# Optimization experiments

Measured on AMD Instinct MI355X. Metric: run time of the kernel, lower is better.

The kernel has to match this reference:

```python
import jax, jax.numpy as jnp
import numpy as np

D = 18          # belief dimension (max category dim)
EPS = 0.1       # C.eps
PROP_STEP = 5   # C.prop_step
CC = 0.01       # label-injection constant c in forward
DIM_A = 4       # category_dim_dict['author']
DIM_P = 18      # category_dim_dict['paper']


def _init_belief(mask, label, dim, d):
    # X[tr_idx] = -c everywhere, then X[tr_idx, label] += dim*c
    m = (mask != 0).astype(jnp.float32)[:, None]            # [N,1]
    X = -CC * m + (dim * CC) * m * jax.nn.one_hot(label, d, dtype=jnp.float32)
    col_mask = (jnp.arange(d) < dim).astype(jnp.float32)    # zero cols >= dim
    Y = X * col_mask
    return X, Y, col_mask


def setup_inputs() -> dict:
    key = jax.random.key(0)
    ks = jax.random.split(key, 8)
    E, NA, NP = 2_000_000, 100_000, 500_000
    return {
        "H_ap": jax.random.normal(ks[0], (D, D), dtype=jnp.float32),
        "H_pa": jax.random.normal(ks[1], (D, D), dtype=jnp.float32),
        "w": jnp.ones((E,), dtype=jnp.float32),
        "edge_src": jax.random.randint(ks[2], (E,), 0, NA, dtype=jnp.int32),
        "edge_dst": jax.random.randint(ks[3], (E,), 0, NP, dtype=jnp.int32),
        "train_mask_a": jax.random.randint(ks[4], (NA,), 0, 2, dtype=jnp.int32),
        "label_a": jax.random.randint(ks[5], (NA,), 0, DIM_A, dtype=jnp.int32),
        "train_mask_p": jax.random.randint(ks[6], (NP,), 0, 2, dtype=jnp.int32),
        "label_p": jax.random.randint(ks[7], (NP,), 0, DIM_P, dtype=jnp.int32),
        "n_author": NA,
        "n_paper": NP,
    }


def reference(H_ap, H_pa, w, edge_src, edge_dst, train_mask_a, label_a,
              train_mask_p, label_p, n_author, n_paper):
    # Belief init via scatter-based label injection (per node type)
    Xa, Ya, cm_a = _init_belief(train_mask_a, label_a, DIM_A, D)
    Xp, Yp, cm_p = _init_belief(train_mask_p, label_p, DIM_P, D)

    seg = jax.ops.segment_sum
    for _ in range(PROP_STEP):  # ZooBP residual updates over hetero edge types
        # author -> paper: gather, transform by H_ap, weighted scatter-add
        msg_p = seg(w[:, None] * (Ya[edge_src] @ H_ap), edge_dst,
                    num_segments=n_paper)                       # [NP, D]
        # paper -> author (inverse etype, H_pa ~ H_ap^T structure)
        msg_a = seg(w[:, None] * (Yp[edge_dst] @ H_pa), edge_src,
                    num_segments=n_author)                      # [NA, D]
        Ya = (Xa + (EPS / D) * msg_a) * cm_a
        Yp = (Xp + (EPS / D) * msg_p) * cm_p
    return Ya, Yp
```

## Files before the change

### kernel.cpp

```cpp
#include <hip/hip_runtime.h>


static constexpr int   DD     = 18;
static constexpr int   DIMA   = 4;
static constexpr float CCF    = 0.01f;
static constexpr float SCALEF = 0.1f / 18.0f;
static constexpr int   PROP   = 5;

static constexpr int NBLK  = 512;
static constexpr int BT    = 512;
static constexpr int PSH   = 10;
static constexpr int ASH   = 9;
static constexpr int PBK   = 512;
static constexpr int ABK   = 256;
static constexpr int PNB   = 1 << PSH;
static constexpr int ANB   = 1 << ASH;
static constexpr int NBIN  = PBK + ABK;
static constexpr int NBINS = NBIN * NBLK;

__device__ __forceinline__ float bf2f(unsigned short u) {
    return __uint_as_float(((unsigned int)u) << 16);
}
__device__ __forceinline__ unsigned short f2bf(float f) {
    unsigned int x = __float_as_uint(f);
    return (unsigned short)((x + 0x7fffu + ((x >> 16) & 1u)) >> 16);
}
__device__ __forceinline__ unsigned int f2w13(float f) {
    unsigned int x = __float_as_uint(f);
    return ((x + 0x3ffffu + ((x >> 19) & 1u)) >> 19) & 0x1fffu;
}
__device__ __forceinline__ float w132f(unsigned int u) {
    return __uint_as_float(u << 19);
}
__device__ __forceinline__ int swz_blk() {
    return ((int)blockIdx.x & 7) * (NBLK >> 3) + ((int)blockIdx.x >> 3);
}

__global__ __launch_bounds__(BT) void count_bins(
    const int* __restrict__ esrc, const int* __restrict__ edst,
    int* __restrict__ bb, int E, int chunk)
{
    __shared__ int hP[PBK];
    __shared__ int hA[ABK];
    int t = threadIdx.x, b = swz_blk();
    if (t < PBK) hP[t] = 0;
    if (t < ABK) hA[t] = 0;
    __syncthreads();
    int beg = b * chunk;
    int end = beg + chunk; if (end > E) end = E;
    for (int e = beg + t; e < end; e += BT) {
        atomicAdd(&hP[edst[e] >> PSH], 1);
        atomicAdd(&hA[esrc[e] >> ASH], 1);
    }
    __syncthreads();
    if (t < PBK) bb[t * NBLK + b] = hP[t];
    if (t < ABK) bb[(PBK + t) * NBLK + b] = hA[t];
}

__global__ __launch_bounds__(256) void scan_block(
    int* __restrict__ off, int* __restrict__ bsum, int NT)
{
    __shared__ int s[256];
    int t = threadIdx.x;
    int i = blockIdx.x * 256 + t;
    int v = (i < NT) ? off[i] : 0;
    s[t] = v; __syncthreads();
    for (int dlt = 1; dlt < 256; dlt <<= 1) {
        int x = (t >= dlt) ? s[t - dlt] : 0;
        __syncthreads();
        s[t] += x;
        __syncthreads();
    }
    if (i < NT) off[i] = s[t] - v;
    if (t == 255) bsum[blockIdx.x] = s[255];
}

__global__ __launch_bounds__(256) void scan_tops(int* __restrict__ bsum, int nb)
{
    __shared__ int s[256];
    int t = threadIdx.x;
    int K = (nb + 255) / 256;
    int base = t * K;
    int sum = 0;
    for (int r = 0; r < K; ++r) { int idx = base + r; if (idx < nb) sum += bsum[idx]; }
    s[t] = sum; __syncthreads();
    for (int dlt = 1; dlt < 256; dlt <<= 1) {
        int x = (t >= dlt) ? s[t - dlt] : 0;
        __syncthreads();
        s[t] += x;
        __syncthreads();
    }
    int run = s[t] - sum;
    for (int r = 0; r < K; ++r) {
        int idx = base + r;
        if (idx < nb) { int tmp = bsum[idx]; bsum[idx] = run; run += tmp; }
    }
}

__global__ __launch_bounds__(BT) void scat_p(
    const int* __restrict__ esrc, const int* __restrict__ edst,
    const float* __restrict__ w, const int* __restrict__ bb,
    const int* __restrict__ bsum, uint2* __restrict__ S, int E, int chunk)
{
    __shared__ int base[PBK];
    int t = threadIdx.x, b = swz_blk();
    if (t < PBK) {
        int idx = t * NBLK + b;
        base[t] = bb[idx] + bsum[idx >> 8];
    }
    __syncthreads();
    int beg = b * chunk;
    int end = beg + chunk; if (end > E) end = E;
    for (int e = beg + t; e < end; e += BT) {
        int d = edst[e], s = esrc[e];
        unsigned int rec = ((unsigned int)s << 13) | f2w13(w[e]);
        int pos = atomicAdd(&base[d >> PSH], 1);
        S[pos] = make_uint2(rec, (unsigned int)(d & (PNB - 1)));
    }
}

__global__ __launch_bounds__(BT) void scat_a(
    const int* __restrict__ esrc, const int* __restrict__ edst,
    const float* __restrict__ w, const int* __restrict__ bb,
    const int* __restrict__ bsum, uint2* __restrict__ S, int E, int chunk,
    int NPH)
{
    __shared__ int base[ABK];
    int t = threadIdx.x, b = swz_blk();
    if (t < ABK) {
        int idx = (PBK + t) * NBLK + b;
        base[t] = bb[idx] + bsum[idx >> 8] - E;
    }
    __syncthreads();
    int beg = b * chunk;
    int end = beg + chunk; if (end > E) end = E;
    for (int e = beg + t; e < end; e += BT) {
        int d = edst[e], s = esrc[e];
        unsigned int rec = ((unsigned int)d << 13) | f2w13(w[e]);
        unsigned int key = ((unsigned int)(s & (ANB - 1)) << 1) | (d >= NPH ? 1u : 0u);
        int pos = atomicAdd(&base[s >> ASH], 1);
        S[pos] = make_uint2(rec, key);
    }
}

__global__ __launch_bounds__(BT) void csr_p(
    const int* __restrict__ bb, const int* __restrict__ bsum,
    const uint2* __restrict__ S,
    unsigned int* __restrict__ adjP, int* __restrict__ offP, int NP, int E)
{
    __shared__ int c[PNB];
    __shared__ int loc[PNB];
    __shared__ int ps[BT];
    int t = threadIdx.x, b = blockIdx.x;
    int i0 = b * NBLK;
    int i1 = (b + 1) * NBLK;
    int sbeg = bb[i0] + bsum[i0 >> 8];
    int send = bb[i1] + bsum[i1 >> 8];
    for (int i = t; i < PNB; i += BT) c[i] = 0;
    __syncthreads();
    for (int i = sbeg + t; i < send; i += BT)
        atomicAdd(&c[S[i].y], 1);
    __syncthreads();
    int a[2]; int sum = 0;
#pragma unroll
    for (int k = 0; k < 2; ++k) { a[k] = c[t * 2 + k]; sum += a[k]; }
    ps[t] = sum; __syncthreads();
    for (int dlt = 1; dlt < BT; dlt <<= 1) {
        int x = (t >= dlt) ? ps[t - dlt] : 0;
        __syncthreads();
        ps[t] += x;
        __syncthreads();
    }
    int run = ps[t] - sum;
    int n0 = (b << PSH) + t * 2;
#pragma unroll
    for (int k = 0; k < 2; ++k) {
        loc[t * 2 + k] = run;
        if (n0 + k < NP) offP[n0 + k] = sbeg + run;
        run += a[k];
    }
    if (b == 0 && t == 0) offP[NP] = E;
    __syncthreads();
    for (int i = sbeg + t; i < send; i += BT) {
        uint2 r = S[i];
        int p = atomicAdd(&loc[r.y], 1);
        adjP[sbeg + p] = r.x;
    }
}

__global__ __launch_bounds__(BT) void csr_a_init(
    const int* __restrict__ bb, const int* __restrict__ bsum,
    const uint2* __restrict__ S,
    unsigned int* __restrict__ adjA, int* __restrict__ offA,
    const int* __restrict__ mask_a, const int* __restrict__ lab_a,
    const int* __restrict__ mask_p, const int* __restrict__ lab_p,
    const float* __restrict__ Hpa,
    ushort4* __restrict__ Ya, ushort4* __restrict__ Zp,
    unsigned char* __restrict__ priorA, unsigned char* __restrict__ priorP,
    int NA, int NTot, int E)
{
    if ((int)blockIdx.x < ABK) {
        __shared__ int c[2 * ANB];
        __shared__ int loc[2 * ANB];
        __shared__ int ps[BT];
        int t = threadIdx.x, b = blockIdx.x;
        int x0 = (PBK + b) * NBLK;
        int sbeg = bb[x0] + bsum[x0 >> 8] - E;
        int send;
        if (b == ABK - 1) send = E;
        else { int x1 = x0 + NBLK; send = bb[x1] + bsum[x1 >> 8] - E; }
        for (int i = t; i < 2 * ANB; i += BT) c[i] = 0;
        __syncthreads();
        for (int i = sbeg + t; i < send; i += BT)
            atomicAdd(&c[S[i].y], 1);
        __syncthreads();
        int a2[2]; int sum = 0;
#pragma unroll
        for (int k = 0; k < 2; ++k) { a2[k] = c[t * 2 + k]; sum += a2[k]; }
        ps[t] = sum; __syncthreads();
        for (int dlt = 1; dlt < BT; dlt <<= 1) {
            int x = (t >= dlt) ? ps[t - dlt] : 0;
            __syncthreads();
            ps[t] += x;
            __syncthreads();
        }
        int run = ps[t] - sum;
        int n0 = (b << (ASH + 1)) + t * 2;
#pragma unroll
        for (int k = 0; k < 2; ++k) {
            loc[t * 2 + k] = run;
            if (n0 + k < 2 * NA) offA[n0 + k] = sbeg + run;
            run += a2[k];
        }
        if (b == 0 && t == 0) offA[2 * NA] = E;
        __syncthreads();
        for (int i = sbeg + t; i < send; i += BT) {
            uint2 r = S[i];
            int p = atomicAdd(&loc[r.y], 1);
            adjA[sbeg + p] = r.x;
        }
    } else {
        __shared__ float sH[72], sCol[4];
        int t = threadIdx.x;
        if (t < 72) sH[t] = Hpa[(t >> 2) * DD + (t & 3)];
        if (t < 4) { float s = 0.f; for (int k = 0; k < DD; ++k) s += Hpa[k * DD + t]; sCol[t] = s; }
        __syncthreads();
        int i = ((int)blockIdx.x - ABK) * BT + t;
        if (i >= NTot) return;
        if (i < NA) {
            float x[4] = {0.f, 0.f, 0.f, 0.f};
            int m = mask_a[i];
            int l = m ? lab_a[i] : 0;
            if (m) {
                x[0] = x[1] = x[2] = x[3] = -CCF;
                x[l] += (float)DIMA * CCF;
            }
            priorA[i] = m ? (unsigned char)(0x20 | l) : 0;
            Ya[i] = make_ushort4(f2bf(x[0]), f2bf(x[1]), f2bf(x[2]), f2bf(x[3]));
        } else {
            int d = i - NA;
            float z0 = 0.f, z1 = 0.f, z2 = 0.f, z3 = 0.f;
            int m = mask_p[d];
            int l = m ? lab_p[d] : 0;
            if (m) {
                float lb = (float)DD * CCF;
                z0 = -CCF * sCol[0] + lb * sH[l * 4 + 0];
                z1 = -CCF * sCol[1] + lb * sH[l * 4 + 1];
                z2 = -CCF * sCol[2] + lb * sH[l * 4 + 2];
                z3 = -CCF * sCol[3] + lb * sH[l * 4 + 3];
            }
            priorP[d] = m ? (unsigned char)(0x20 | l) : 0;
            Zp[d] = make_ushort4(f2bf(z0), f2bf(z1), f2bf(z2), f2bf(z3));
        }
    }
}

__global__ __launch_bounds__(256) void gather_iter(
    const int* __restrict__ offP, const int* __restrict__ offA,
    const unsigned int* __restrict__ adjP, const unsigned int* __restrict__ adjA,
    const ushort4* __restrict__ ZpOld, ushort4* __restrict__ ZpNew,
    const ushort4* __restrict__ YaOld, ushort4* __restrict__ YaNew,
    const unsigned char* __restrict__ priorA, const unsigned char* __restrict__ priorP,
    const float* __restrict__ Hap, const float* __restrict__ Hpa,
    float* __restrict__ out, int NP, int NA, int last, int gpB)
{
    if ((int)blockIdx.x < gpB) {
        __shared__ float sH[72], sCol[4], sM[16], sHap[72];
        int t = threadIdx.x;
        if (t < 72) sH[t] = Hpa[(t >> 2) * DD + (t & 3)];
        if (t < 4) { float s = 0.f; for (int k = 0; k < DD; ++k) s += Hpa[k * DD + t]; sCol[t] = s; }
        if (t < 16) { int i = t >> 2, j = t & 3; float s = 0.f;
                      for (int k = 0; k < DD; ++k) s += Hap[i * DD + k] * Hpa[k * DD + j];
                      sM[t] = SCALEF * s; }
        if (t < 72) sHap[t] = SCALEF * Hap[t];
        __syncthreads();

        int d = (int)blockIdx.x * 256 + t;
        if (d >= NP) return;
        int beg = offP[d], end = offP[d + 1];
        unsigned int pb = priorP[d];
        float ax = 0.f, ay = 0.f, az = 0.f, aw = 0.f;
        int s = beg;
        for (; s + 8 <= end; s += 8) {
            unsigned int e0 = adjP[s],     e1 = adjP[s + 1], e2 = adjP[s + 2], e3 = adjP[s + 3];
            unsigned int e4 = adjP[s + 4], e5 = adjP[s + 5], e6 = adjP[s + 6], e7 = adjP[s + 7];
            ushort4 y0 = YaOld[e0 >> 13], y1 = YaOld[e1 >> 13];
            ushort4 y2 = YaOld[e2 >> 13], y3 = YaOld[e3 >> 13];
            ushort4 y4 = YaOld[e4 >> 13], y5 = YaOld[e5 >> 13];
            ushort4 y6 = YaOld[e6 >> 13], y7 = YaOld[e7 >> 13];
            float w0 = w132f(e0 & 0x1fffu), w1 = w132f(e1 & 0x1fffu);
            float w2 = w132f(e2 & 0x1fffu), w3 = w132f(e3 & 0x1fffu);
            float w4 = w132f(e4 & 0x1fffu), w5 = w132f(e5 & 0x1fffu);
            float w6 = w132f(e6 & 0x1fffu), w7 = w132f(e7 & 0x1fffu);
            ax += w0 * bf2f(y0.x) + w1 * bf2f(y1.x) + w2 * bf2f(y2.x) + w3 * bf2f(y3.x)
                + w4 * bf2f(y4.x) + w5 * bf2f(y5.x) + w6 * bf2f(y6.x) + w7 * bf2f(y7.x);
            ay += w0 * bf2f(y0.y) + w1 * bf2f(y1.y) + w2 * bf2f(y2.y) + w3 * bf2f(y3.y)
                + w4 * bf2f(y4.y) + w5 * bf2f(y5.y) + w6 * bf2f(y6.y) + w7 * bf2f(y7.y);
            az += w0 * bf2f(y0.z) + w1 * bf2f(y1.z) + w2 * bf2f(y2.z) + w3 * bf2f(y3.z)
                + w4 * bf2f(y4.z) + w5 * bf2f(y5.z) + w6 * bf2f(y6.z) + w7 * bf2f(y7.z);
            aw += w0 * bf2f(y0.w) + w1 * bf2f(y1.w) + w2 * bf2f(y2.w) + w3 * bf2f(y3.w)
                + w4 * bf2f(y4.w) + w5 * bf2f(y5.w) + w6 * bf2f(y6.w) + w7 * bf2f(y7.w);
        }
        for (; s + 4 <= end; s += 4) {
            unsigned int e0 = adjP[s], e1 = adjP[s + 1], e2 = adjP[s + 2], e3 = adjP[s + 3];
            ushort4 y0 = YaOld[e0 >> 13], y1 = YaOld[e1 >> 13];
            ushort4 y2 = YaOld[e2 >> 13], y3 = YaOld[e3 >> 13];
            float w0 = w132f(e0 & 0x1fffu), w1 = w132f(e1 & 0x1fffu);
            float w2 = w132f(e2 & 0x1fffu), w3 = w132f(e3 & 0x1fffu);
            ax += w0 * bf2f(y0.x) + w1 * bf2f(y1.x) + w2 * bf2f(y2.x) + w3 * bf2f(y3.x);
            ay += w0 * bf2f(y0.y) + w1 * bf2f(y1.y) + w2 * bf2f(y2.y) + w3 * bf2f(y3.y);
            az += w0 * bf2f(y0.z) + w1 * bf2f(y1.z) + w2 * bf2f(y2.z) + w3 * bf2f(y3.z);
            aw += w0 * bf2f(y0.w) + w1 * bf2f(y1.w) + w2 * bf2f(y2.w) + w3 * bf2f(y3.w);
        }
        for (; s < end; ++s) {
            unsigned int ent = adjP[s];
            float wt = w132f(ent & 0x1fffu);
            ushort4 yv = YaOld[ent >> 13];
            ax += wt * bf2f(yv.x); ay += wt * bf2f(yv.y);
            az += wt * bf2f(yv.z); aw += wt * bf2f(yv.w);
        }
        int l = pb & 31;
        float base = pb ? -CCF : 0.f;
        float lb   = pb ? (float)DD * CCF : 0.f;
        if (!last) {
            float z0 = base * sCol[0] + lb * sH[l * 4 + 0] + ax * sM[0] + ay * sM[4] + az * sM[8]  + aw * sM[12];
            float z1 = base * sCol[1] + lb * sH[l * 4 + 1] + ax * sM[1] + ay * sM[5] + az * sM[9]  + aw * sM[13];
            float z2 = base * sCol[2] + lb * sH[l * 4 + 2] + ax * sM[2] + ay * sM[6] + az * sM[10] + aw * sM[14];
            float z3 = base * sCol[3] + lb * sH[l * 4 + 3] + ax * sM[3] + ay * sM[7] + az * sM[11] + aw * sM[15];
            ZpNew[d] = make_ushort4(f2bf(z0), f2bf(z1), f2bf(z2), f2bf(z3));
        } else {
            float* row = out + (size_t)(NA + d) * DD;
#pragma unroll
            for (int j = 0; j < DD; ++j) {
                row[j] = base + ((j == l) ? lb : 0.f)
                       + ax * sHap[0 * DD + j] + ay * sHap[1 * DD + j]
                       + az * sHap[2 * DD + j] + aw * sHap[3 * DD + j];
            }
        }
    } else {
        int tid = ((int)blockIdx.x - gpB) * 256 + threadIdx.x;
        int a = tid >> 2, sub = tid & 3;
        if (a >= NA) return;
        int beg = offA[2 * a], mid = offA[2 * a + 1], end = offA[2 * a + 2];
        unsigned int pb = priorA[a];
        float ax = 0.f, ay = 0.f, az = 0.f, aw = 0.f;
#pragma unroll
        for (int h = 0; h < 2; ++h) {
            int lo = h ? mid : beg;
            int hi = h ? end : mid;
            int s = lo + sub;
            for (; s + 4 < hi; s += 8) {
                unsigned int e0 = adjA[s], e1 = adjA[s + 4];
                ushort4 z0 = ZpOld[e0 >> 13], z1 = ZpOld[e1 >> 13];
                float w0 = w132f(e0 & 0x1fffu), w1 = w132f(e1 & 0x1fffu);
                ax += w0 * bf2f(z0.x) + w1 * bf2f(z1.x);
                ay += w0 * bf2f(z0.y) + w1 * bf2f(z1.y);
                az += w0 * bf2f(z0.z) + w1 * bf2f(z1.z);
                aw += w0 * bf2f(z0.w) + w1 * bf2f(z1.w);
            }
            for (; s < hi; s += 4) {
                unsigned int ent = adjA[s];
                float wt = w132f(ent & 0x1fffu);
                ushort4 z = ZpOld[ent >> 13];
                ax += wt * bf2f(z.x); ay += wt * bf2f(z.y);
                az += wt * bf2f(z.z); aw += wt * bf2f(z.w);
            }
        }
        ax += __shfl_xor(ax, 1); ay += __shfl_xor(ay, 1);
        az += __shfl_xor(az, 1); aw += __shfl_xor(aw, 1);
        ax += __shfl_xor(ax, 2); ay += __shfl_xor(ay, 2);
        az += __shfl_xor(az, 2); aw += __shfl_xor(aw, 2);
        if (sub == 0) {
            int l = pb & 31;
            float x0 = pb ? ((l == 0) ? ((float)DIMA - 1.f) * CCF : -CCF) : 0.f;
            float x1 = pb ? ((l == 1) ? ((float)DIMA - 1.f) * CCF : -CCF) : 0.f;
            float x2 = pb ? ((l == 2) ? ((float)DIMA - 1.f) * CCF : -CCF) : 0.f;
            float x3 = pb ? ((l == 3) ? ((float)DIMA - 1.f) * CCF : -CCF) : 0.f;
            float y0 = x0 + SCALEF * ax, y1 = x1 + SCALEF * ay;
            float y2 = x2 + SCALEF * az, y3 = x3 + SCALEF * aw;
            YaNew[a] = make_ushort4(f2bf(y0), f2bf(y1), f2bf(y2), f2bf(y3));
            if (last) {
                float* row = out + (size_t)a * DD;
                row[0] = y0; row[1] = y1; row[2] = y2; row[3] = y3;
#pragma unroll
                for (int j = DIMA; j < DD; ++j) row[j] = 0.f;
            }
        }
    }
}

extern "C" void kernel_launch(void* const* d_in, const int* in_sizes, int n_in,
                              void* d_out, int out_size, void* d_ws, size_t ws_size,
                              hipStream_t stream)
{
    const float* H_ap   = (const float*)d_in[0];
    const float* H_pa   = (const float*)d_in[1];
    const float* w      = (const float*)d_in[2];
    const int*   esrc   = (const int*)d_in[3];
    const int*   edst   = (const int*)d_in[4];
    const int*   mask_a = (const int*)d_in[5];
    const int*   lab_a  = (const int*)d_in[6];
    const int*   mask_p = (const int*)d_in[7];
    const int*   lab_p  = (const int*)d_in[8];

    const int E  = in_sizes[2];
    const int NA = in_sizes[5];
    const int NP = in_sizes[7];
    const int NT = NP + NA;
    const int NPH = NP / 2;

    char*  basep = (char*)d_ws;
    size_t o = 0;
    auto alloc = [&](size_t bytes) -> char* {
        o = (o + 15) & ~(size_t)15;
        char* p = basep + o;
        o += bytes;
        return p;
    };
    int*           offP   = (int*)          alloc((size_t)(NP + 1) * sizeof(int));
    int*           offA   = (int*)          alloc((size_t)(2 * NA + 1) * sizeof(int));
    int*           bb     = (int*)          alloc((size_t)(NBINS + 1) * sizeof(int));
    int*           bsum   = (int*)          alloc((size_t)4096 * sizeof(int));
    unsigned int*  adjP   = (unsigned int*) alloc((size_t)E * sizeof(unsigned int));
    unsigned int*  adjA   = (unsigned int*) alloc((size_t)E * sizeof(unsigned int));
    unsigned char* priorP = (unsigned char*)alloc((size_t)NP);
    unsigned char* priorA = (unsigned char*)alloc((size_t)NA);
    ushort4*       YaA    = (ushort4*)      alloc((size_t)NA * sizeof(ushort4));
    ushort4*       YaB    = (ushort4*)      alloc((size_t)NA * sizeof(ushort4));
    ushort4*       ZpA    = (ushort4*)      alloc((size_t)NP * sizeof(ushort4));
    (void)ws_size;

    float*   out = (float*)d_out;
    uint2*   S   = (uint2*)d_out;
    size_t   sBytes = (((size_t)E * sizeof(uint2)) + 255) & ~(size_t)255;
    ushort4* ZpB = (ushort4*)((char*)d_out + sBytes);

    ushort4* YaBuf[2] = {YaA, YaB};
    ushort4* ZpBuf[2] = {ZpA, ZpB};

    const int chunk = (E + NBLK - 1) / NBLK;
    const int gp    = (NP + 255) / 256;
    const int ga4   = (NA * 4 + 255) / 256;
    const int gni   = (NT + BT - 1) / BT;
    const int nb    = (NBINS + 255) / 256;

    count_bins<<<NBLK, BT, 0, stream>>>(esrc, edst, bb, E, chunk);
    scan_block<<<nb, 256, 0, stream>>>(bb, bsum, NBINS);
    scan_tops<<<1, 256, 0, stream>>>(bsum, nb);
    scat_p<<<NBLK, BT, 0, stream>>>(esrc, edst, w, bb, bsum, S, E, chunk);
    csr_p<<<PBK, BT, 0, stream>>>(bb, bsum, S, adjP, offP, NP, E);
    scat_a<<<NBLK, BT, 0, stream>>>(esrc, edst, w, bb, bsum, S, E, chunk, NPH);
    csr_a_init<<<ABK + gni, BT, 0, stream>>>(bb, bsum, S, adjA, offA,
                                             mask_a, lab_a, mask_p, lab_p, H_pa,
                                             YaA, ZpA, priorA, priorP,
                                             NA, NT, E);

    for (int it = 0; it < PROP; ++it) {
        int last = (it == PROP - 1) ? 1 : 0;
        int cur = it & 1, nxt = 1 - cur;
        gather_iter<<<gp + ga4, 256, 0, stream>>>(offP, offA, adjP, adjA,
                                                  ZpBuf[cur], ZpBuf[nxt],
                                                  YaBuf[cur], YaBuf[nxt],
                                                  priorA, priorP,
                                                  H_ap, H_pa, out,
                                                  NP, NA, last, gp);
    }
}
```

Measured before the change: 336.3 us.

## Fuse paper and author scatter and CSR builds; use 8 lanes per author gather

```diff
diff --git a/kernel.cpp b/kernel.cpp
--- a/kernel.cpp
+++ b/kernel.cpp
@@ -97,113 +97,88 @@
     }
 }
 
-__global__ __launch_bounds__(BT) void scat_p(
+__global__ __launch_bounds__(BT) void scat_pa(
     const int* __restrict__ esrc, const int* __restrict__ edst,
     const float* __restrict__ w, const int* __restrict__ bb,
-    const int* __restrict__ bsum, uint2* __restrict__ S, int E, int chunk)
-{
-    __shared__ int base[PBK];
+    const int* __restrict__ bsum,
+    uint2* __restrict__ S_p, uint2* __restrict__ S_a,
+    int E, int chunk, int NPH)
+{
+    __shared__ int baseP[PBK];
+    __shared__ int baseA[ABK];
     int t = threadIdx.x, b = swz_blk();
     if (t < PBK) {
         int idx = t * NBLK + b;
-        base[t] = bb[idx] + bsum[idx >> 8];
+        baseP[t] = bb[idx] + bsum[idx >> 8];
+    }
+    if (t < ABK) {
+        int idx = (PBK + t) * NBLK + b;
+        baseA[t] = bb[idx] + bsum[idx >> 8] - E;
     }
     __syncthreads();
     int beg = b * chunk;
     int end = beg + chunk; if (end > E) end = E;
     for (int e = beg + t; e < end; e += BT) {
         int d = edst[e], s = esrc[e];
-        unsigned int rec = ((unsigned int)s << 13) | f2w13(w[e]);
-        int pos = atomicAdd(&base[d >> PSH], 1);
-        S[pos] = make_uint2(rec, (unsigned int)(d & (PNB - 1)));
-    }
-}
-
-__global__ __launch_bounds__(BT) void scat_a(
-    const int* __restrict__ esrc, const int* __restrict__ edst,
-    const float* __restrict__ w, const int* __restrict__ bb,
-    const int* __restrict__ bsum, uint2* __restrict__ S, int E, int chunk,
-    int NPH)
-{
-    __shared__ int base[ABK];
-    int t = threadIdx.x, b = swz_blk();
-    if (t < ABK) {
-        int idx = (PBK + t) * NBLK + b;
-        base[t] = bb[idx] + bsum[idx >> 8] - E;
-    }
-    __syncthreads();
-    int beg = b * chunk;
-    int end = beg + chunk; if (end > E) end = E;
-    for (int e = beg + t; e < end; e += BT) {
-        int d = edst[e], s = esrc[e];
-        unsigned int rec = ((unsigned int)d << 13) | f2w13(w[e]);
+        unsigned int w13 = f2w13(w[e]);
+        int posP = atomicAdd(&baseP[d >> PSH], 1);
+        S_p[posP] = make_uint2(((unsigned int)s << 13) | w13,
+                               (unsigned int)(d & (PNB - 1)));
         unsigned int key = ((unsigned int)(s & (ANB - 1)) << 1) | (d >= NPH ? 1u : 0u);
-        int pos = atomicAdd(&base[s >> ASH], 1);
-        S[pos] = make_uint2(rec, key);
-    }
-}
-
-__global__ __launch_bounds__(BT) void csr_p(
+        int posA = atomicAdd(&baseA[s >> ASH], 1);
+        S_a[posA] = make_uint2(((unsigned int)d << 13) | w13, key);
+    }
+}
+
+__global__ __launch_bounds__(BT) void csr_all(
     const int* __restrict__ bb, const int* __restrict__ bsum,
-    const uint2* __restrict__ S,
-    unsigned int* __restrict__ adjP, int* __restrict__ offP, int NP, int E)
-{
-    __shared__ int c[PNB];
-    __shared__ int loc[PNB];
-    __shared__ int ps[BT];
-    int t = threadIdx.x, b = blockIdx.x;
-    int i0 = b * NBLK;
-    int i1 = (b + 1) * NBLK;
-    int sbeg = bb[i0] + bsum[i0 >> 8];
-    int send = bb[i1] + bsum[i1 >> 8];
-    for (int i = t; i < PNB; i += BT) c[i] = 0;
-    __syncthreads();
-    for (int i = sbeg + t; i < send; i += BT)
-        atomicAdd(&c[S[i].y], 1);
-    __syncthreads();
-    int a[2]; int sum = 0;
-#pragma unroll
-    for (int k = 0; k < 2; ++k) { a[k] = c[t * 2 + k]; sum += a[k]; }
-    ps[t] = sum; __syncthreads();
-    for (int dlt = 1; dlt < BT; dlt <<= 1) {
-        int x = (t >= dlt) ? ps[t - dlt] : 0;
-        __syncthreads();
-        ps[t] += x;
-        __syncthreads();
-    }
-    int run = ps[t] - sum;
-    int n0 = (b << PSH) + t * 2;
-#pragma unroll
-    for (int k = 0; k < 2; ++k) {
-        loc[t * 2 + k] = run;
-        if (n0 + k < NP) offP[n0 + k] = sbeg + run;
-        run += a[k];
-    }
-    if (b == 0 && t == 0) offP[NP] = E;
-    __syncthreads();
-    for (int i = sbeg + t; i < send; i += BT) {
-        uint2 r = S[i];
-        int p = atomicAdd(&loc[r.y], 1);
-        adjP[sbeg + p] = r.x;
-    }
-}
-
-__global__ __launch_bounds__(BT) void csr_a_init(
-    const int* __restrict__ bb, const int* __restrict__ bsum,
-    const uint2* __restrict__ S,
+    const uint2* __restrict__ S_p, const uint2* __restrict__ S_a,
+    unsigned int* __restrict__ adjP, int* __restrict__ offP,
     unsigned int* __restrict__ adjA, int* __restrict__ offA,
     const int* __restrict__ mask_a, const int* __restrict__ lab_a,
     const int* __restrict__ mask_p, const int* __restrict__ lab_p,
     const float* __restrict__ Hpa,
     ushort4* __restrict__ Ya, ushort4* __restrict__ Zp,
     unsigned char* __restrict__ priorA, unsigned char* __restrict__ priorP,
-    int NA, int NTot, int E)
-{
-    if ((int)blockIdx.x < ABK) {
-        __shared__ int c[2 * ANB];
-        __shared__ int loc[2 * ANB];
-        __shared__ int ps[BT];
+    int NP, int NA, int NTot, int E)
+{
+    __shared__ int c[PNB];
+    __shared__ int loc[PNB];
+    __shared__ int ps[BT];
+    if ((int)blockIdx.x < PBK) {
         int t = threadIdx.x, b = blockIdx.x;
+        int i0 = b * NBLK;
+        int i1 = (b + 1) * NBLK;
+        int sbeg = bb[i0] + bsum[i0 >> 8];
+        int send = bb[i1] + bsum[i1 >> 8];
+        for (int i = t; i < PNB; i += BT) c[i] = 0;
+        __syncthreads();
+        for (int i = sbeg + t; i < send; i += BT)
+            atomicAdd(&c[S_p[i].y], 1);
+        __syncthreads();
+        int a0 = c[2 * t], a1 = c[2 * t + 1];
+        ps[t] = a0 + a1; __syncthreads();
+        for (int dlt = 1; dlt < BT; dlt <<= 1) {
+            int x = (t >= dlt) ? ps[t - dlt] : 0;
+            __syncthreads();
+            ps[t] += x;
+            __syncthreads();
+        }
+        int run = ps[t] - a0 - a1;
+        int n0 = (b << PSH) + 2 * t;
+        loc[2 * t] = run;
+        loc[2 * t + 1] = run + a0;
+        if (n0 < NP)     offP[n0]     = sbeg + run;
+        if (n0 + 1 < NP) offP[n0 + 1] = sbeg + run + a0;
+        if (b == 0 && t == 0) offP[NP] = E;
+        __syncthreads();
+        for (int i = sbeg + t; i < send; i += BT) {
+            uint2 r = S_p[i];
+            int p = atomicAdd(&loc[r.y], 1);
+            adjP[sbeg + p] = r.x;
+        }
+    } else if ((int)blockIdx.x < PBK + ABK) {
+        int t = threadIdx.x, b = (int)blockIdx.x - PBK;
         int x0 = (PBK + b) * NBLK;
         int sbeg = bb[x0] + bsum[x0 >> 8] - E;
         int send;
@@ -212,30 +187,26 @@
         for (int i = t; i < 2 * ANB; i += BT) c[i] = 0;
         __syncthreads();
         for (int i = sbeg + t; i < send; i += BT)
-            atomicAdd(&c[S[i].y], 1);
-        __syncthreads();
-        int a2[2]; int sum = 0;
-#pragma unroll
-        for (int k = 0; k < 2; ++k) { a2[k] = c[t * 2 + k]; sum += a2[k]; }
-        ps[t] = sum; __syncthreads();
+            atomicAdd(&c[S_a[i].y], 1);
+        __syncthreads();
+        int a0 = c[2 * t], a1 = c[2 * t + 1];
+        ps[t] = a0 + a1; __syncthreads();
         for (int dlt = 1; dlt < BT; dlt <<= 1) {
             int x = (t >= dlt) ? ps[t - dlt] : 0;
             __syncthreads();
             ps[t] += x;
             __syncthreads();
         }
-        int run = ps[t] - sum;
-        int n0 = (b << (ASH + 1)) + t * 2;
-#pragma unroll
-        for (int k = 0; k < 2; ++k) {
-            loc[t * 2 + k] = run;
-            if (n0 + k < 2 * NA) offA[n0 + k] = sbeg + run;
-            run += a2[k];
-        }
+        int run = ps[t] - a0 - a1;
+        int n0 = (b << (ASH + 1)) + 2 * t;
+        loc[2 * t] = run;
+        loc[2 * t + 1] = run + a0;
+        if (n0 < 2 * NA)     offA[n0]     = sbeg + run;
+        if (n0 + 1 < 2 * NA) offA[n0 + 1] = sbeg + run + a0;
         if (b == 0 && t == 0) offA[2 * NA] = E;
         __syncthreads();
         for (int i = sbeg + t; i < send; i += BT) {
-            uint2 r = S[i];
+            uint2 r = S_a[i];
             int p = atomicAdd(&loc[r.y], 1);
             adjA[sbeg + p] = r.x;
         }
@@ -245,7 +216,7 @@
         if (t < 72) sH[t] = Hpa[(t >> 2) * DD + (t & 3)];
         if (t < 4) { float s = 0.f; for (int k = 0; k < DD; ++k) s += Hpa[k * DD + t]; sCol[t] = s; }
         __syncthreads();
-        int i = ((int)blockIdx.x - ABK) * BT + t;
+        int i = ((int)blockIdx.x - PBK - ABK) * BT + t;
         if (i >= NTot) return;
         if (i < NA) {
             float x[4] = {0.f, 0.f, 0.f, 0.f};
@@ -359,7 +330,7 @@
         }
     } else {
         int tid = ((int)blockIdx.x - gpB) * 256 + threadIdx.x;
-        int a = tid >> 2, sub = tid & 3;
+        int a = tid >> 3, sub = tid & 7;
         if (a >= NA) return;
         int beg = offA[2 * a], mid = offA[2 * a + 1], end = offA[2 * a + 2];
         unsigned int pb = priorA[a];
@@ -369,8 +340,8 @@
             int lo = h ? mid : beg;
             int hi = h ? end : mid;
             int s = lo + sub;
-            for (; s + 4 < hi; s += 8) {
-                unsigned int e0 = adjA[s], e1 = adjA[s + 4];
+            for (; s + 8 < hi; s += 16) {
+                unsigned int e0 = adjA[s], e1 = adjA[s + 8];
                 ushort4 z0 = ZpOld[e0 >> 13], z1 = ZpOld[e1 >> 13];
                 float w0 = w132f(e0 & 0x1fffu), w1 = w132f(e1 & 0x1fffu);
                 ax += w0 * bf2f(z0.x) + w1 * bf2f(z1.x);
@@ -378,7 +349,7 @@
                 az += w0 * bf2f(z0.z) + w1 * bf2f(z1.z);
                 aw += w0 * bf2f(z0.w) + w1 * bf2f(z1.w);
             }
-            for (; s < hi; s += 4) {
+            for (; s < hi; s += 8) {
                 unsigned int ent = adjA[s];
                 float wt = w132f(ent & 0x1fffu);
                 ushort4 z = ZpOld[ent >> 13];
@@ -390,6 +361,8 @@
         az += __shfl_xor(az, 1); aw += __shfl_xor(aw, 1);
         ax += __shfl_xor(ax, 2); ay += __shfl_xor(ay, 2);
         az += __shfl_xor(az, 2); aw += __shfl_xor(aw, 2);
+        ax += __shfl_xor(ax, 4); ay += __shfl_xor(ay, 4);
+        az += __shfl_xor(az, 4); aw += __shfl_xor(aw, 4);
         if (sub == 0) {
             int l = pb & 31;
             float x0 = pb ? ((l == 0) ? ((float)DIMA - 1.f) * CCF : -CCF) : 0.f;
@@ -451,34 +424,35 @@
     (void)ws_size;
 
     float*   out = (float*)d_out;
-    uint2*   S   = (uint2*)d_out;
     size_t   sBytes = (((size_t)E * sizeof(uint2)) + 255) & ~(size_t)255;
-    ushort4* ZpB = (ushort4*)((char*)d_out + sBytes);
+    uint2*   S_p = (uint2*)d_out;
+    uint2*   S_a = (uint2*)((char*)d_out + sBytes);
+    ushort4* ZpB = (ushort4*)((char*)d_out + 2 * sBytes);
 
     ushort4* YaBuf[2] = {YaA, YaB};
     ushort4* ZpBuf[2] = {ZpA, ZpB};
 
     const int chunk = (E + NBLK - 1) / NBLK;
     const int gp    = (NP + 255) / 256;
-    const int ga4   = (NA * 4 + 255) / 256;
+    const int ga8   = (NA * 8 + 255) / 256;
     const int gni   = (NT + BT - 1) / BT;
     const int nb    = (NBINS + 255) / 256;
 
     count_bins<<<NBLK, BT, 0, stream>>>(esrc, edst, bb, E, chunk);
     scan_block<<<nb, 256, 0, stream>>>(bb, bsum, NBINS);
     scan_tops<<<1, 256, 0, stream>>>(bsum, nb);
-    scat_p<<<NBLK, BT, 0, stream>>>(esrc, edst, w, bb, bsum, S, E, chunk);
-    csr_p<<<PBK, BT, 0, stream>>>(bb, bsum, S, adjP, offP, NP, E);
-    scat_a<<<NBLK, BT, 0, stream>>>(esrc, edst, w, bb, bsum, S, E, chunk, NPH);
-    csr_a_init<<<ABK + gni, BT, 0, stream>>>(bb, bsum, S, adjA, offA,
-                                             mask_a, lab_a, mask_p, lab_p, H_pa,
-                                             YaA, ZpA, priorA, priorP,
-                                             NA, NT, E);
+    scat_pa<<<NBLK, BT, 0, stream>>>(esrc, edst, w, bb, bsum, S_p, S_a,
+                                     E, chunk, NPH);
+    csr_all<<<PBK + ABK + gni, BT, 0, stream>>>(bb, bsum, S_p, S_a,
+                                                adjP, offP, adjA, offA,
+                                                mask_a, lab_a, mask_p, lab_p,
+                                                H_pa, YaA, ZpA, priorA, priorP,
+                                                NP, NA, NT, E);
 
     for (int it = 0; it < PROP; ++it) {
         int last = (it == PROP - 1) ? 1 : 0;
         int cur = it & 1, nxt = 1 - cur;
-        gather_iter<<<gp + ga4, 256, 0, stream>>>(offP, offA, adjP, adjA,
+        gather_iter<<<gp + ga8, 256, 0, stream>>>(offP, offA, adjP, adjA,
                                                   ZpBuf[cur], ZpBuf[nxt],
                                                   YaBuf[cur], YaBuf[nxt],
                                                   priorA, priorP,
```

Measured after the change: 341.5 us. About the same (+1.6%).
